# Kernel optimization log

Hardware: AMD Instinct MI355X
Metric: run time of the kernel (lower is better)

## Reference

```python
import jax, jax.numpy as jnp
import numpy as np

MARGIN = 0.3  # init_kwargs
EPS = 1e-12   # torch F.normalize eps


def _pairwise_dist(f):
    # Euclidean cdist via the stable quadratic expansion; f is [B, D].
    sq = jnp.sum(f * f, axis=1)                      # [B]
    d2 = sq[:, None] + sq[None, :] - 2.0 * (f @ f.T)  # [B, B]
    d2 = jnp.maximum(d2, 0.0)
    # safe sqrt: zero distance (diagonal / duplicates) -> 0 with zero grad
    pos = d2 > 0.0
    return jnp.sqrt(jnp.where(pos, d2, 1.0)) * pos


def reference(features, labels):
    B = features.shape[0]
    norm = jnp.linalg.norm(features, axis=1, keepdims=True)
    f = features / jnp.maximum(norm, EPS)            # F.normalize(dim=1)

    dist = _pairwise_dist(f)                         # [B, B]
    mask = labels[:, None] == labels[None, :]        # positives (incl. self)

    pos_count = jnp.sum(mask, axis=1)                # [B], >= 1 (self)
    has_pos = pos_count > 1                          # needs another positive
    has_neg = pos_count < B                          # at least one negative
    valid = has_pos & has_neg

    # mean over positive distances (includes the self-distance 0, as in torch code)
    mean_pos = jnp.sum(dist * mask, axis=1) / pos_count.astype(dist.dtype)  # [B]

    # semi-hard negatives: negatives with dist > mean positive dist
    sh_mask = (~mask) & (dist > mean_pos[:, None])   # [B, B]
    has_sh = jnp.any(sh_mask, axis=1)
    min_sh = jnp.min(jnp.where(sh_mask, dist, jnp.inf), axis=1)
    min_sh = jnp.where(has_sh, min_sh, 0.0)          # guard inf for invalid rows

    contrib = valid & has_sh
    per_anchor = jax.nn.relu(mean_pos - min_sh + MARGIN)
    loss_sum = jnp.sum(jnp.where(contrib, per_anchor, 0.0))
    count = jnp.sum(contrib)
    return jnp.where(count > 0, loss_sum / count.astype(dist.dtype), 0.0)


def setup_inputs() -> dict:
    key = jax.random.key(0)
    k1, k2 = jax.random.split(key)
    features = jax.random.normal(k1, (8192, 512), dtype=jnp.float32)
    labels = jax.random.randint(k2, (8192,), 0, 128, dtype=jnp.int64)
    return {"features": features, "labels": labels}
```

## Files before the change

kernel.cpp:

```cpp
#include <hip/hip_runtime.h>
#include <math.h>

#define EPS_N 1e-12f
#define MARGIN 0.3f
#define INF_BITS 0x7f800000u
#define NCLS 128
#define D 512
#define PADR 256

typedef __attribute__((ext_vector_type(8))) short short8;
typedef __attribute__((ext_vector_type(4))) float float4v;

__device__ __forceinline__ unsigned short f2bf(float f) {
    unsigned u = __float_as_uint(f);
    u += 0x7fff + ((u >> 16) & 1);
    return (unsigned short)(u >> 16);
}
__device__ __forceinline__ void gl16(const void* g, void* l) {
    __builtin_amdgcn_global_load_lds((const __attribute__((address_space(1))) void*)g,
                                     (__attribute__((address_space(3))) void*)l, 16, 0, 0);
}

__global__ __launch_bounds__(1024) void k_bucket(const int* __restrict__ lab, int Bn,
        int* __restrict__ pos, int* __restrict__ labp,
        int* __restrict__ cstart_g, int* __restrict__ ccnt_g,
        float* __restrict__ meanpos, float* __restrict__ pcinv,
        int* __restrict__ poscnt, unsigned* __restrict__ minbits) {
    __shared__ int cnt[NCLS], cs[NCLS + 1], off[NCLS], sa[NCLS], sb[NCLS];
    int tid = threadIdx.x;
    if (tid < NCLS) cnt[tid] = 0;
    __syncthreads();
    for (int i = tid; i < Bn; i += 1024) atomicAdd(&cnt[lab[i] & (NCLS - 1)], 1);
    __syncthreads();
    if (tid < NCLS) sa[tid] = cnt[tid];
    __syncthreads();
    int* src = sa; int* dst = sb;
    for (int ofs = 1; ofs < NCLS; ofs <<= 1) {
        if (tid < NCLS) dst[tid] = src[tid] + ((tid >= ofs) ? src[tid - ofs] : 0);
        __syncthreads();
        int* t = src; src = dst; dst = t;
    }
    if (tid < NCLS) {
        int ex = src[tid] - cnt[tid];
        cs[tid] = ex;
        off[tid] = ex;
        cstart_g[tid] = ex;
        ccnt_g[tid] = cnt[tid];
    }
    if (tid == 0) cs[NCLS] = Bn;
    __syncthreads();
    for (int p = tid; p < Bn; p += 1024) {
        int lo = 0, hi = NCLS - 1;
        #pragma unroll
        for (int s = 0; s < 7; ++s) {
            int mid = (lo + hi + 1) >> 1;
            if (cs[mid] <= p) lo = mid; else hi = mid - 1;
        }
        int l = lo, m = cnt[l];
        labp[p] = l;
        poscnt[p] = m;
        pcinv[p] = 1.0f / (float)m;
        meanpos[p] = 0.f;
        minbits[p] = INF_BITS;
    }
    for (int i = tid; i < Bn; i += 1024) {
        int l = lab[i] & (NCLS - 1);
        pos[i] = atomicAdd(&off[l], 1);
    }
}

__global__ __launch_bounds__(256) void k_normalize(const float* __restrict__ x,
        const int* __restrict__ pos, unsigned short* __restrict__ fh,
        float* __restrict__ sqp) {
    int w = threadIdx.x >> 6, L = threadIdx.x & 63;
    int row = blockIdx.x * 4 + w;
    const float* xr = x + (size_t)row * D + L * 8;
    float4 a = *(const float4*)xr;
    float4 b = *(const float4*)(xr + 4);
    float ss = a.x * a.x;
    ss = fmaf(a.y, a.y, ss); ss = fmaf(a.z, a.z, ss); ss = fmaf(a.w, a.w, ss);
    ss = fmaf(b.x, b.x, ss); ss = fmaf(b.y, b.y, ss);
    ss = fmaf(b.z, b.z, ss); ss = fmaf(b.w, b.w, ss);
    #pragma unroll
    for (int off = 32; off; off >>= 1) ss += __shfl_xor(ss, off, 64);
    float inv = 1.0f / fmaxf(sqrtf(ss), EPS_N);
    int prow = pos[row];
    if (L == 0) sqp[prow] = ss * inv * inv;
    ushort4 h0, h1;
    h0.x = f2bf(a.x * inv); h0.y = f2bf(a.y * inv);
    h0.z = f2bf(a.z * inv); h0.w = f2bf(a.w * inv);
    h1.x = f2bf(b.x * inv); h1.y = f2bf(b.y * inv);
    h1.z = f2bf(b.z * inv); h1.w = f2bf(b.w * inv);
    unsigned short* dst = fh + (size_t)prow * D + L * 8;
    *(ushort4*)dst = h0;
    *(ushort4*)(dst + 4) = h1;
}

__global__ __launch_bounds__(256) void k_posclass(
    const unsigned short* __restrict__ fh, const float* __restrict__ sqp,
    const int* __restrict__ cstart_g, const int* __restrict__ ccnt_g,
    float* __restrict__ meanpos)
{
    const int c = blockIdx.x;
    const int s = cstart_g[c], n = ccnt_g[c];
    if (n <= 1) return;

    __shared__ unsigned short SA[128 * 128];
    __shared__ unsigned short SB[128 * 128];
    __shared__ float sqr_sh[128], sqs[128], rs[128];

    const int tid = threadIdx.x, w = tid >> 6, L = tid & 63;
    const int lm = L & 15, ls = L >> 4;

    for (int rb = 0; rb < n; rb += 128) {
        const int nr = min(128, n - rb);
        __syncthreads();
        if (tid < 128) {
            rs[tid] = 0.f;
            sqr_sh[tid] = (tid < nr) ? sqp[s + rb + tid] : 0.f;
        }
        for (int cb = 0; cb < n; cb += 128) {
            const int m = min(128, n - cb);
            const bool same = (rb == cb);
            __syncthreads();
            if (tid < 128) sqs[tid] = (tid < m) ? sqp[s + cb + tid] : 0.f;

            float4v acc[8][2];
            #pragma unroll
            for (int rt = 0; rt < 8; ++rt)
                #pragma unroll
                for (int ct = 0; ct < 2; ++ct) acc[rt][ct] = (float4v){0.f, 0.f, 0.f, 0.f};

            for (int k0 = 0; k0 < D; k0 += 128) {
                __syncthreads();
                #pragma unroll
                for (int q = 0; q < 8; ++q) {
                    int slot = tid + 256 * q;
                    int r = slot >> 4;
                    int u = (slot & 15) ^ (r & 15);
                    if (r < nr)
                        gl16(fh + (size_t)(s + rb + r) * D + k0 + u * 8,
                             &SA[(w * 64 + 256 * q) * 8]);
                }
                if (!same) {
                    #pragma unroll
                    for (int q = 0; q < 8; ++q) {
                        int slot = tid + 256 * q;
                        int r = slot >> 4;
                        int u = (slot & 15) ^ (r & 15);
                        if (r < m)
                            gl16(fh + (size_t)(s + cb + r) * D + k0 + u * 8,
                                 &SB[(w * 64 + 256 * q) * 8]);
                    }
                }
                __syncthreads();
                const unsigned short* Bb = same ? SA : SB;
                #pragma unroll
                for (int h = 0; h < 4; ++h) {
                    short8 bf[2];
                    #pragma unroll
                    for (int ct = 0; ct < 2; ++ct) {
                        int cr = w * 32 + ct * 16 + lm;
                        bf[ct] = *(const short8*)&Bb[cr * 128 + (((h * 4 + ls) ^ (cr & 15))) * 8];
                    }
                    #pragma unroll
                    for (int rt = 0; rt < 8; ++rt) {
                        int ar = rt * 16 + lm;
                        short8 af = *(const short8*)&SA[ar * 128 + (((h * 4 + ls) ^ (ar & 15))) * 8];
                        #pragma unroll
                        for (int ct = 0; ct < 2; ++ct)
                            acc[rt][ct] = __builtin_amdgcn_mfma_f32_16x16x32_bf16(af, bf[ct], acc[rt][ct], 0, 0, 0);
                    }
                }
            }
            #pragma unroll
            for (int rt = 0; rt < 8; ++rt) {
                #pragma unroll
                for (int v = 0; v < 4; ++v) {
                    int ri = rt * 16 + ls * 4 + v;
                    float sr = sqr_sh[ri];
                    float sum = 0.f;
                    #pragma unroll
                    for (int ct = 0; ct < 2; ++ct) {
                        int ci = w * 32 + ct * 16 + lm;
                        float d2 = sr + sqs[ci] - 2.0f * acc[rt][ct][v];
                        bool ok = (ri < nr) && (ci < m) && (rb + ri != cb + ci) && (d2 > 0.f);
                        sum += ok ? sqrtf(d2) : 0.f;
                    }
                    #pragma unroll
                    for (int off = 8; off; off >>= 1) sum += __shfl_xor(sum, off, 64);
                    if (lm == 0 && sum != 0.f) atomicAdd(&rs[ri], sum);
                }
            }
        }
        __syncthreads();
        if (tid < nr) meanpos[s + rb + tid] = rs[tid];
    }
}

#define BKG 64

__global__ __launch_bounds__(256, 4) void k_minsh_mfma(
    const unsigned short* __restrict__ fh, const float* __restrict__ sqp,
    const int* __restrict__ labp, const float* __restrict__ meanpos,
    const float* __restrict__ pcinv, unsigned* __restrict__ minbits)
{
    int t = blockIdx.x;
    int rq = (int)((sqrtf(8.0f * (float)t + 1.0f) - 1.0f) * 0.5f);
    while ((rq + 1) * (rq + 2) / 2 <= t) ++rq;
    while (rq * (rq + 1) / 2 > t) --rq;
    int cq = t - rq * (rq + 1) / 2;
    const int i0 = cq * 128, j0 = rq * 128;
    const bool diag = (i0 == j0);

    __shared__ unsigned short LA[2][128 * BKG];
    __shared__ float s_mp2r[128], s_mp2c[128], s_sqr[128], s_sqc[128];
    __shared__ int s_labr[128], s_labc[128];

    const int tid = threadIdx.x;
    const int w = tid >> 6, L = tid & 63;

    if (tid < 128) {
        float mp = meanpos[i0 + tid] * pcinv[i0 + tid];
        s_mp2r[tid] = mp * mp;
        s_sqr[tid]  = sqp[i0 + tid];
        s_labr[tid] = labp[i0 + tid];
    } else {
        int q = tid - 128;
        float mp = meanpos[j0 + q] * pcinv[j0 + q];
        s_mp2c[q] = mp * mp;
        s_sqc[q]  = sqp[j0 + q];
        s_labc[q] = labp[j0 + q];
    }

    const unsigned short* msrc = fh + (size_t)((w < 2) ? i0 : j0) * D;
    unsigned short* mylds = &LA[(w < 2) ? 0 : 1][(w & 1) * 64 * BKG];
    const int srow = L >> 3;
    const int sseg = L & 7;

    float4v acc[4][4];
    #pragma unroll
    for (int a = 0; a < 4; ++a)
        #pragma unroll
        for (int bq = 0; bq < 4; ++bq) acc[a][bq] = (float4v){0.f, 0.f, 0.f, 0.f};

    const int rw = (w >> 1) * 64, cw = (w & 1) * 64;
    const int lm = L & 15, ls = L >> 4;

    for (int k0 = 0; k0 < D; k0 += BKG) {
        __syncthreads();
        #pragma unroll
        for (int it = 0; it < 8; ++it) {
            int rmat = (w & 1) * 64 + it * 8 + srow;
            int seg = sseg ^ (rmat & 7);
            gl16(msrc + (size_t)rmat * D + k0 + seg * 8, mylds + it * 512);
        }
        __syncthreads();
        #pragma unroll
        for (int h = 0; h < 2; ++h) {
            short8 ah[4], bh[4];
            #pragma unroll
            for (int mi = 0; mi < 4; ++mi) {
                int r = rw + mi * 16 + lm;
                int slot = r * 8 + ((h * 4 + ls) ^ (r & 7));
                ah[mi] = *(const short8*)&LA[0][slot * 8];
            }
            #pragma unroll
            for (int ni = 0; ni < 4; ++ni) {
                int cc = cw + ni * 16 + lm;
                int slot = cc * 8 + ((h * 4 + ls) ^ (cc & 7));
                bh[ni] = *(const short8*)&LA[1][slot * 8];
            }
            #pragma unroll
            for (int ni = 0; ni < 4; ++ni)
                #pragma unroll
                for (int mi = 0; mi < 4; ++mi)
                    acc[mi][ni] = __builtin_amdgcn_mfma_f32_16x16x32_bf16(ah[mi], bh[ni], acc[mi][ni], 0, 0, 0);
        }
    }

    const float INFF = __uint_as_float(INF_BITS);
    float sc[4], mp2c[4];
    int lc[4];
    #pragma unroll
    for (int ni = 0; ni < 4; ++ni) {
        int cl = cw + ni * 16 + lm;
        sc[ni]   = s_sqc[cl];
        mp2c[ni] = s_mp2c[cl];
        lc[ni]   = s_labc[cl];
    }
    float vminc[4];
    #pragma unroll
    for (int ni = 0; ni < 4; ++ni) vminc[ni] = INFF;

    #pragma unroll
    for (int mi = 0; mi < 4; ++mi) {
        #pragma unroll
        for (int v = 0; v < 4; ++v) {
            int rl = rw + mi * 16 + ls * 4 + v;
            float mp2r = s_mp2r[rl];
            float sr   = s_sqr[rl];
            int   li   = s_labr[rl];
            float vminr = INFF;
            #pragma unroll
            for (int ni = 0; ni < 4; ++ni) {
                float d2 = fmaf(-2.0f, acc[mi][ni][v], sr + sc[ni]);
                bool neq = (li != lc[ni]);
                vminr     = fminf(vminr,     (neq && d2 > mp2r)     ? d2 : INFF);
                vminc[ni] = fminf(vminc[ni], (neq && d2 > mp2c[ni]) ? d2 : INFF);
            }
            #pragma unroll
            for (int off = 8; off; off >>= 1)
                vminr = fminf(vminr, __shfl_xor(vminr, off, 64));
            if (lm == 0 && __float_as_uint(vminr) != INF_BITS)
                atomicMin(&minbits[i0 + rl], __float_as_uint(vminr));
        }
    }
    if (!diag) {
        #pragma unroll
        for (int ni = 0; ni < 4; ++ni) {
            float vc = vminc[ni];
            vc = fminf(vc, __shfl_xor(vc, 16, 64));
            vc = fminf(vc, __shfl_xor(vc, 32, 64));
            if (ls == 0 && __float_as_uint(vc) != INF_BITS)
                atomicMin(&minbits[j0 + cw + ni * 16 + lm], __float_as_uint(vc));
        }
    }
}

__global__ __launch_bounds__(1024) void k_finish(const float* __restrict__ meanpos,
        const float* __restrict__ pcinv, const int* __restrict__ poscnt,
        const unsigned* __restrict__ minbits, float* __restrict__ out, int Bn) {
    float lsum = 0.f; int lcnt = 0;
    for (int i = threadIdx.x; i < Bn; i += 1024) {
        int pc = poscnt[i];
        bool valid = (pc > 1) && (pc < Bn);
        unsigned mb = minbits[i];
        if (valid && mb != INF_BITS) {
            float v = fmaf(meanpos[i], pcinv[i], MARGIN - sqrtf(__uint_as_float(mb)));
            lsum += (v > 0.f) ? v : 0.f;
            lcnt += 1;
        }
    }
    __shared__ float ssum[16]; __shared__ int scnt[16];
    int lane = threadIdx.x & 63, wid = threadIdx.x >> 6;
    #pragma unroll
    for (int off = 32; off; off >>= 1) {
        lsum += __shfl_down(lsum, off, 64);
        lcnt += __shfl_down(lcnt, off, 64);
    }
    if (lane == 0) { ssum[wid] = lsum; scnt[wid] = lcnt; }
    __syncthreads();
    if (threadIdx.x == 0) {
        float s = 0.f; int c = 0;
        #pragma unroll
        for (int q = 0; q < 16; ++q) { s += ssum[q]; c += scnt[q]; }
        out[0] = (c > 0) ? s / (float)c : 0.f;
    }
}

extern "C" void kernel_launch(void* const* d_in, const int* in_sizes, int n_in,
                              void* d_out, int out_size, void* d_ws, size_t ws_size,
                              hipStream_t stream) {
    const float* x = (const float*)d_in[0];
    const int* lab = (const int*)d_in[1];
    int Bn = in_sizes[1];

    size_t nd = (size_t)(Bn + PADR) * D;
    unsigned short* fh = (unsigned short*)d_ws;
    float* sqp        = (float*)(fh + nd);
    float* meanpos    = sqp + Bn;
    float* pcinv      = meanpos + Bn;
    int* poscnt       = (int*)(pcinv + Bn);
    unsigned* minbits = (unsigned*)(poscnt + Bn);
    int* pos          = (int*)(minbits + Bn);
    int* labp         = pos + Bn;
    int* cstart_g     = labp + Bn;
    int* ccnt_g       = cstart_g + NCLS;

    k_bucket<<<1, 1024, 0, stream>>>(lab, Bn, pos, labp, cstart_g, ccnt_g,
                                     meanpos, pcinv, poscnt, minbits);
    k_normalize<<<Bn / 4, 256, 0, stream>>>(x, pos, fh, sqp);
    k_posclass<<<NCLS, 256, 0, stream>>>(fh, sqp, cstart_g, ccnt_g, meanpos);
    int nb = Bn / 128;
    int T = nb * (nb + 1) / 2;
    k_minsh_mfma<<<T, 256, 0, stream>>>(fh, sqp, labp, meanpos, pcinv, minbits);
    k_finish<<<1, 1024, 0, stream>>>(meanpos, pcinv, poscnt, minbits,
                                     (float*)d_out, Bn);
}
```

Before: 159.1 us.

## Load MFMA operands directly from global memory and remap block order

Removes LDS staging of the feature tiles in the min-semi-hard kernel. Each lane now loads its bf16 MFMA operand fragments straight from global memory (L2/L1) with no per-k-step barriers, which also frees the LDS that capped occupancy. Block indices are permuted in strides of 260 across the triangular tile schedule, likely to spread work or improve L2 locality across XCDs. Operands are no longer shared inside the block, so global and cache traffic goes up and each fragment read is a strided 16-byte access.

```diff
diff --git a/kernel.cpp b/kernel.cpp
--- a/kernel.cpp
+++ b/kernel.cpp
@@ -198,14 +198,12 @@
     }
 }
 
-#define BKG 64
-
 __global__ __launch_bounds__(256, 4) void k_minsh_mfma(
     const unsigned short* __restrict__ fh, const float* __restrict__ sqp,
     const int* __restrict__ labp, const float* __restrict__ meanpos,
     const float* __restrict__ pcinv, unsigned* __restrict__ minbits)
 {
-    int t = blockIdx.x;
+    int t = (blockIdx.x & 7) * 260 + (blockIdx.x >> 3);
     int rq = (int)((sqrtf(8.0f * (float)t + 1.0f) - 1.0f) * 0.5f);
     while ((rq + 1) * (rq + 2) / 2 <= t) ++rq;
     while (rq * (rq + 1) / 2 > t) --rq;
@@ -213,12 +211,13 @@
     const int i0 = cq * 128, j0 = rq * 128;
     const bool diag = (i0 == j0);
 
-    __shared__ unsigned short LA[2][128 * BKG];
     __shared__ float s_mp2r[128], s_mp2c[128], s_sqr[128], s_sqc[128];
     __shared__ int s_labr[128], s_labc[128];
 
     const int tid = threadIdx.x;
     const int w = tid >> 6, L = tid & 63;
+    const int lm = L & 15, ls = L >> 4;
+    const int rw = (w >> 1) * 64, cw = (w & 1) * 64;
 
     if (tid < 128) {
         float mp = meanpos[i0 + tid] * pcinv[i0 + tid];
@@ -233,10 +232,8 @@
         s_labc[q] = labp[j0 + q];
     }
 
-    const unsigned short* msrc = fh + (size_t)((w < 2) ? i0 : j0) * D;
-    unsigned short* mylds = &LA[(w < 2) ? 0 : 1][(w & 1) * 64 * BKG];
-    const int srow = L >> 3;
-    const int sseg = L & 7;
+    const unsigned short* pa = fh + (size_t)(i0 + rw + lm) * D + ls * 8;
+    const unsigned short* pb = fh + (size_t)(j0 + cw + lm) * D + ls * 8;
 
     float4v acc[4][4];
     #pragma unroll
@@ -244,40 +241,22 @@
         #pragma unroll
         for (int bq = 0; bq < 4; ++bq) acc[a][bq] = (float4v){0.f, 0.f, 0.f, 0.f};
 
-    const int rw = (w >> 1) * 64, cw = (w & 1) * 64;
-    const int lm = L & 15, ls = L >> 4;
-
-    for (int k0 = 0; k0 < D; k0 += BKG) {
-        __syncthreads();
-        #pragma unroll
-        for (int it = 0; it < 8; ++it) {
-            int rmat = (w & 1) * 64 + it * 8 + srow;
-            int seg = sseg ^ (rmat & 7);
-            gl16(msrc + (size_t)rmat * D + k0 + seg * 8, mylds + it * 512);
-        }
-        __syncthreads();
-        #pragma unroll
-        for (int h = 0; h < 2; ++h) {
-            short8 ah[4], bh[4];
-            #pragma unroll
-            for (int mi = 0; mi < 4; ++mi) {
-                int r = rw + mi * 16 + lm;
-                int slot = r * 8 + ((h * 4 + ls) ^ (r & 7));
-                ah[mi] = *(const short8*)&LA[0][slot * 8];
-            }
-            #pragma unroll
-            for (int ni = 0; ni < 4; ++ni) {
-                int cc = cw + ni * 16 + lm;
-                int slot = cc * 8 + ((h * 4 + ls) ^ (cc & 7));
-                bh[ni] = *(const short8*)&LA[1][slot * 8];
-            }
-            #pragma unroll
-            for (int ni = 0; ni < 4; ++ni)
-                #pragma unroll
-                for (int mi = 0; mi < 4; ++mi)
-                    acc[mi][ni] = __builtin_amdgcn_mfma_f32_16x16x32_bf16(ah[mi], bh[ni], acc[mi][ni], 0, 0, 0);
-        }
-    }
+    #pragma unroll 2
+    for (int kt = 0; kt < 16; ++kt) {
+        short8 ah[4], bh[4];
+        #pragma unroll
+        for (int mi = 0; mi < 4; ++mi)
+            ah[mi] = *(const short8*)(pa + mi * 16 * D + kt * 32);
+        #pragma unroll
+        for (int ni = 0; ni < 4; ++ni)
+            bh[ni] = *(const short8*)(pb + ni * 16 * D + kt * 32);
+        #pragma unroll
+        for (int ni = 0; ni < 4; ++ni)
+            #pragma unroll
+            for (int mi = 0; mi < 4; ++mi)
+                acc[mi][ni] = __builtin_amdgcn_mfma_f32_16x16x32_bf16(ah[mi], bh[ni], acc[mi][ni], 0, 0, 0);
+    }
+    __syncthreads();
 
     const float INFF = __uint_as_float(INF_BITS);
     float sc[4], mp2c[4];
```

After: 237.5 us. 49.2% more time.
